# Kernel tuning notes

Measured on AMD Instinct MI355X. Metric: run time of the kernel, lower is better.

Reference implementation:

```python
import jax, jax.numpy as jnp
import numpy as np

B, C, H, W = 8, 256, 64, 64
CI = 128  # inter_channels = in_channels // reduction

def _conv1x1(x, w, b):
    # x: [b, c, h, w], w: [o, c], b: [o]
    return jnp.einsum('bchw,oc->bohw', x, w) + b[None, :, None, None]

def setup_inputs() -> dict:
    key = jax.random.key(0)
    ks = jax.random.split(key, 5)
    s_in = 1.0 / np.sqrt(C)
    s_ci = 1.0 / np.sqrt(CI)
    return {
        'x': jax.random.normal(ks[0], (B, C, H, W), jnp.float32),
        'w_g': jax.random.normal(ks[1], (CI, C), jnp.float32) * s_in,
        'b_g': jnp.zeros((CI,), jnp.float32),
        'w_theta': jax.random.normal(ks[2], (CI, C), jnp.float32) * s_in,
        'b_theta': jnp.zeros((CI,), jnp.float32),
        'w_phi': jax.random.normal(ks[3], (CI, C), jnp.float32) * s_in,
        'b_phi': jnp.zeros((CI,), jnp.float32),
        'w_out': jax.random.normal(ks[4], (C, CI), jnp.float32) * s_ci,
        'b_out': jnp.zeros((C,), jnp.float32),
    }

def reference(x, w_g, b_g, w_theta, b_theta, w_phi, b_phi, w_out, b_out):
    n, c, h, w = x.shape
    N = h * w
    g_x = _conv1x1(x, w_g, b_g).reshape(n, CI, N).transpose(0, 2, 1)        # [b, N, ci]
    theta_x = _conv1x1(x, w_theta, b_theta).reshape(n, CI, N).transpose(0, 2, 1)  # [b, N, ci]
    phi_x = _conv1x1(x, w_phi, b_phi).reshape(n, CI, N)                     # [b, ci, N]
    pw = jnp.einsum('bnc,bcm->bnm', theta_x, phi_x)                         # [b, N, N]
    # Faithful to source: divides by ci**(-0.5) == multiplies by sqrt(ci)
    pw = pw / (jnp.asarray(CI, x.dtype) ** -0.5)
    pw = jax.nn.softmax(pw, axis=-1)
    y = jnp.einsum('bnm,bmc->bnc', pw, g_x)                                 # [b, N, ci]
    y = y.transpose(0, 2, 1).reshape(n, CI, h, w)
    return x + _conv1x1(y, w_out, b_out)
```

## Files before the change

### kernel.cpp

```cpp
#include <hip/hip_runtime.h>
#include <hip/hip_bf16.h>
#include <stdint.h>
#include <stddef.h>


typedef __bf16 bf16;
typedef __attribute__((ext_vector_type(8))) __bf16 bf16x8;
typedef __attribute__((ext_vector_type(4))) __bf16 bf16x4;
typedef __attribute__((ext_vector_type(4))) float  f32x4;
typedef __attribute__((ext_vector_type(4))) int    i32x4;

#define MFMA16(a, b, c) __builtin_amdgcn_mfma_f32_16x16x32_bf16((a), (b), (c), 0, 0, 0)

__device__ __forceinline__ void gload_lds16(const void* g, void* l) {
    __builtin_amdgcn_global_load_lds(
        (const __attribute__((address_space(1))) void*)g,
        (__attribute__((address_space(3))) void*)l, 16, 0, 0);
}

constexpr int NB  = 8;
constexpr int NC  = 256;
constexpr int NN  = 4096;
constexpr int NCI = 128;
constexpr size_t NEL = (size_t)NB * NN * NCI;
constexpr int PBATCH = NN * NCI;

#define QSCALE (11.313708498984761f * 1.4426950408889634f)


__global__ __launch_bounds__(256) void k_proj3(
    const float* __restrict__ x,
    const float* __restrict__ wt, const float* __restrict__ bt,
    const float* __restrict__ wp, const float* __restrict__ bp,
    const float* __restrict__ wg, const float* __restrict__ bg,
    const float* __restrict__ wo, bf16* __restrict__ wob,
    bf16* __restrict__ qh, bf16* __restrict__ ql,
    bf16* __restrict__ kh, bf16* __restrict__ kl,
    bf16* __restrict__ vv)
{
    const int nt  = blockIdx.x;
    const int b   = blockIdx.y;
    const int tid = threadIdx.x;
    const int wv  = tid >> 6;
    const int ln  = tid & 63;
    const int lg  = ln >> 4;
    const int lq  = ln & 15;

    if (wob != nullptr && tid < 16) {
        int idx = (b * 64 + nt) * 64 + tid * 4;
        f32x4 w4 = *(const f32x4*)(wo + idx);
        bf16x4 o4;
#pragma unroll
        for (int e = 0; e < 4; ++e) o4[e] = (bf16)w4[e];
        *(bf16x4*)(wob + idx) = o4;
    }

    __shared__ char lds[49152];
    char* Ah = lds;
    char* Al = lds + 8192;
    char* Wh = lds + 16384;
    char* Wl = lds + 32768;

    f32x4 acc[3][8];
#pragma unroll
    for (int pj = 0; pj < 3; ++pj)
#pragma unroll
        for (int j = 0; j < 8; ++j) acc[pj][j] = f32x4{0.f, 0.f, 0.f, 0.f};

    const int n0 = nt * 64;

    for (int c0 = 0; c0 < NC; c0 += 64) {
        __syncthreads();
#pragma unroll
        for (int p = 0; p < 4; ++p) {
            int cc = p * 16 + (tid >> 4);
            int nn = (tid & 15) * 4;
            f32x4 xv = *(const f32x4*)(x + ((size_t)b * NC + (c0 + cc)) * NN + n0 + nn);
#pragma unroll
            for (int e = 0; e < 4; ++e) {
                float f = xv[e];
                bf16 hh = (bf16)f;
                int row = nn + e;
                int off = (row * 128 + cc * 2) ^ ((row & 7) << 4);
                *(bf16*)(Ah + off) = hh;
                *(bf16*)(Al + off) = (bf16)(f - (float)hh);
            }
        }

#pragma unroll
        for (int pj = 0; pj < 3; ++pj) {
            const float* W = (pj == 0) ? wt : (pj == 1) ? wp : wg;
            const bool split = (pj != 2);
            if (pj != 0) __syncthreads();
#pragma unroll
            for (int p = 0; p < 8; ++p) {
                int i  = p * 16 + (tid >> 4);
                int c4 = (tid & 15) * 4;
                f32x4 w4 = *(const f32x4*)(W + (size_t)i * NC + c0 + c4);
                bf16x4 hv, lv;
#pragma unroll
                for (int e = 0; e < 4; ++e) {
                    bf16 hh = (bf16)w4[e];
                    hv[e] = hh;
                    lv[e] = (bf16)(w4[e] - (float)hh);
                }
                int off = (i * 128 + c4 * 2) ^ ((i & 7) << 4);
                *(bf16x4*)(Wh + off) = hv;
                if (split) *(bf16x4*)(Wl + off) = lv;
            }
            __syncthreads();
#pragma unroll
            for (int kk = 0; kk < 2; ++kk) {
                int row  = wv * 16 + lq;
                int koff = kk * 64 + lg * 16;
                int aoff = (row * 128 + koff) ^ ((row & 7) << 4);
                bf16x8 ah = *(const bf16x8*)(Ah + aoff);
                bf16x8 al = *(const bf16x8*)(Al + aoff);
#pragma unroll
                for (int j = 0; j < 8; ++j) {
                    int ir   = j * 16 + lq;
                    int woff = (ir * 128 + koff) ^ ((ir & 7) << 4);
                    bf16x8 bh = *(const bf16x8*)(Wh + woff);
                    acc[pj][j] = MFMA16(ah, bh, acc[pj][j]);
                    if (split) {
                        bf16x8 bl = *(const bf16x8*)(Wl + woff);
                        acc[pj][j] = MFMA16(ah, bl, acc[pj][j]);
                        acc[pj][j] = MFMA16(al, bh, acc[pj][j]);
                    }
                }
            }
        }
    }

#pragma unroll
    for (int j = 0; j < 8; ++j) {
        int i = j * 16 + lq;
        float bvt = bt[i];
        float bvp = bp[i];
#pragma unroll
        for (int r = 0; r < 4; ++r) {
            int q = n0 + wv * 16 + lg * 4 + r;
            size_t off = ((size_t)b * NN + q) * NCI + i;
            float vt2 = (acc[0][j][r] + bvt) * QSCALE;
            bf16 th = (bf16)vt2;
            qh[off] = th; ql[off] = (bf16)(vt2 - (float)th);
            float vp2 = acc[1][j][r] + bvp;
            bf16 phh = (bf16)vp2;
            size_t ko = (size_t)b * PBATCH + (size_t)(q >> 5) * 4096
                      + (size_t)((q & 31) * 128 + (((i >> 3) ^ (q & 7)) << 3) + (i & 7));
            kh[ko] = phh; kl[ko] = (bf16)(vp2 - (float)phh);
        }
    }

    __syncthreads();
    char* T = lds;
#pragma unroll
    for (int j = 0; j < 8; ++j) {
        int i = j * 16 + lq;
        float bv2 = bg[i];
#pragma unroll
        for (int r = 0; r < 4; ++r) {
            int nl = wv * 16 + lg * 4 + r;
            int off = (i * 128 + nl * 2) ^ ((i & 7) << 4);
            *(bf16*)(T + off) = (bf16)(acc[2][j][r] + bv2);
        }
    }
    __syncthreads();
#pragma unroll
    for (int p = 0; p < 4; ++p) {
        int i  = p * 32 + (tid >> 3);
        int sl = tid & 7;
        i32x4 tv = *(const i32x4*)(T + ((i * 128 + sl * 16) ^ ((i & 7) << 4)));
        size_t off = (size_t)b * PBATCH
                   + (size_t)((((nt * 8 + (i >> 4)) * 2 + (sl >> 2)) * 64
                               + (sl & 3) * 16 + (i & 15)) * 8);
        *(i32x4*)(vv + off) = tv;
    }
}

__global__ __launch_bounds__(128, 2) void k_attn_sp(
    const bf16* __restrict__ qh, const bf16* __restrict__ ql,
    const bf16* __restrict__ khp, const bf16* __restrict__ klp,
    const bf16* __restrict__ vf,
    bf16* __restrict__ p0, bf16* __restrict__ p1, float* __restrict__ ml)
{
    const int bid = blockIdx.x;
    const int b   = bid & 7;
    const int rs  = bid >> 3;
    const int qt  = rs & 63;
    const int h   = rs >> 6;
    const int tid = threadIdx.x;
    const int wv  = tid >> 6;
    const int ln  = tid & 63;
    const int lg  = ln >> 4;
    const int lq  = ln & 15;
    const int n0  = qt * 64;
    bf16* ph = h ? p1 : p0;

    __shared__ __attribute__((aligned(16))) char lds[36864];
    char* P = lds + 32768 + wv * 2048;

    const bf16* ksh = khp + (size_t)b * PBATCH + wv * 2048 + (size_t)ln * 8;
    const bf16* ksl = klp + (size_t)b * PBATCH + wv * 2048 + (size_t)ln * 8;

    bf16x8 qhf[2][4], qlf[2][4];
#pragma unroll
    for (int q2 = 0; q2 < 2; ++q2) {
        int qrow = n0 + wv * 32 + q2 * 16 + lq;
        const bf16* bh = qh + ((size_t)b * NN + qrow) * NCI;
        const bf16* bl = ql + ((size_t)b * NN + qrow) * NCI;
#pragma unroll
        for (int kk = 0; kk < 4; ++kk) {
            qhf[q2][kk] = *(const bf16x8*)(bh + kk * 32 + lg * 8);
            qlf[q2][kk] = *(const bf16x8*)(bl + kk * 32 + lg * 8);
        }
    }

    f32x4 o[2][8];
#pragma unroll
    for (int q2 = 0; q2 < 2; ++q2)
#pragma unroll
        for (int j = 0; j < 8; ++j) o[q2][j] = f32x4{0.f, 0.f, 0.f, 0.f};
    float mrun[2] = {-1e30f, -1e30f};
    float lrun[2] = {0.f, 0.f};

    const bf16* vb = vf + (size_t)b * PBATCH + (size_t)ln * 8;

    {
        const bf16* sh = ksh + (size_t)(h * 64) * 4096;
        const bf16* sl = ksl + (size_t)(h * 64) * 4096;
        char* dh = lds + wv * 4096;
        char* dl = lds + 8192 + wv * 4096;
#pragma unroll
        for (int c = 0; c < 4; ++c) {
            gload_lds16(sh + c * 512, dh + c * 1024);
            gload_lds16(sl + c * 512, dl + c * 1024);
        }
    }
    __syncthreads();

    for (int t = 0; t < 64; ++t) {
        const int cur = t & 1;
        char* KHc = lds + cur * 16384;
        char* KLc = KHc + 8192;
        char* KHn = lds + (cur ^ 1) * 16384;
        char* KLn = KHn + 8192;
        const bool pre = (t < 63);

        if (pre) {
            const bf16* sh = ksh + (size_t)(h * 64 + t + 1) * 4096;
            const bf16* sl = ksl + (size_t)(h * 64 + t + 1) * 4096;
            char* dh = KHn + wv * 4096;
            char* dl = KLn + wv * 4096;
#pragma unroll
            for (int c = 0; c < 4; ++c) {
                gload_lds16(sh + c * 512, dh + c * 1024);
                gload_lds16(sl + c * 512, dl + c * 1024);
            }
        }
        __builtin_amdgcn_sched_barrier(0);

        f32x4 s[2][2];
        __builtin_amdgcn_s_setprio(1);
#pragma unroll
        for (int jm = 0; jm < 2; ++jm) {
            s[jm][0] = f32x4{0.f, 0.f, 0.f, 0.f};
            s[jm][1] = f32x4{0.f, 0.f, 0.f, 0.f};
            const int mrow = jm * 16 + lq;
            const int sw = (mrow & 7) << 4;
#pragma unroll
            for (int kk = 0; kk < 4; ++kk) {
                int aoff = (mrow * 256 + kk * 64 + lg * 16) ^ sw;
                bf16x8 ah = *(const bf16x8*)(KHc + aoff);
                bf16x8 al = *(const bf16x8*)(KLc + aoff);
                s[jm][0] = MFMA16(ah, qhf[0][kk], s[jm][0]);
                s[jm][1] = MFMA16(ah, qhf[1][kk], s[jm][1]);
                s[jm][0] = MFMA16(al, qhf[0][kk], s[jm][0]);
                s[jm][1] = MFMA16(al, qhf[1][kk], s[jm][1]);
                s[jm][0] = MFMA16(ah, qlf[0][kk], s[jm][0]);
                s[jm][1] = MFMA16(ah, qlf[1][kk], s[jm][1]);
            }
        }
        __builtin_amdgcn_s_setprio(0);

        bf16x8 bv[8];
        {
            const bf16* vp = vb + (size_t)(h * 32 + (t >> 1)) * 8192;
#pragma unroll
            for (int j = 0; j < 8; ++j)
                bv[j] = *(const bf16x8*)(vp + (j * 2 + (t & 1)) * 512);
        }
        __builtin_amdgcn_sched_barrier(0);

        float tm[2];
        tm[0] = s[0][0][0];
        tm[1] = s[0][1][0];
#pragma unroll
        for (int jm = 0; jm < 2; ++jm)
#pragma unroll
            for (int r = 0; r < 4; ++r) {
                tm[0] = fmaxf(tm[0], s[jm][0][r]);
                tm[1] = fmaxf(tm[1], s[jm][1][r]);
            }
#pragma unroll
        for (int q2 = 0; q2 < 2; ++q2) {
            tm[q2] = fmaxf(tm[q2], __shfl_xor(tm[q2], 16));
            tm[q2] = fmaxf(tm[q2], __shfl_xor(tm[q2], 32));
        }

        bool grow = (tm[0] > mrun[0] + 8.f) || (tm[1] > mrun[1] + 8.f);
        if (__any(grow)) {
            float alpha[2];
#pragma unroll
            for (int q2 = 0; q2 < 2; ++q2) {
                float mnew = fmaxf(mrun[q2], tm[q2]);
                alpha[q2] = exp2f(mrun[q2] - mnew);
                mrun[q2] = mnew;
                lrun[q2] *= alpha[q2];
            }
            float av0[4], av1[4];
#pragma unroll
            for (int r = 0; r < 4; ++r) {
                av0[r] = __shfl(alpha[0], lg * 4 + r);
                av1[r] = __shfl(alpha[1], lg * 4 + r);
            }
#pragma unroll
            for (int j = 0; j < 8; ++j)
#pragma unroll
                for (int r = 0; r < 4; ++r) {
                    o[0][j][r] *= av0[r];
                    o[1][j][r] *= av1[r];
                }
        }

        float psum[2] = {0.f, 0.f};
#pragma unroll
        for (int jm = 0; jm < 2; ++jm)
#pragma unroll
            for (int q2 = 0; q2 < 2; ++q2) {
                bf16x4 pk;
#pragma unroll
                for (int r = 0; r < 4; ++r) {
                    float e2 = exp2f(s[jm][q2][r] - mrun[q2]);
                    psum[q2] += e2;
                    pk[r] = (bf16)e2;
                }
                int row = q2 * 16 + lq;
                int off = (row * 64 + (jm * 16 + lg * 4) * 2) ^ ((row & 7) << 4);
                *(bf16x4*)(P + off) = pk;
            }
#pragma unroll
        for (int q2 = 0; q2 < 2; ++q2) {
            psum[q2] += __shfl_xor(psum[q2], 16);
            psum[q2] += __shfl_xor(psum[q2], 32);
            lrun[q2] += psum[q2];
        }

        bf16x8 pa[2];
#pragma unroll
        for (int q2 = 0; q2 < 2; ++q2) {
            int row = q2 * 16 + lq;
            pa[q2] = *(const bf16x8*)(P + ((row * 64 + lg * 16) ^ ((row & 7) << 4)));
        }
        __builtin_amdgcn_s_setprio(1);
#pragma unroll
        for (int j = 0; j < 8; ++j) {
            o[0][j] = MFMA16(pa[0], bv[j], o[0][j]);
            o[1][j] = MFMA16(pa[1], bv[j], o[1][j]);
        }
        __builtin_amdgcn_s_setprio(0);

        __syncthreads();
    }

    float rl0[4], rl1[4];
#pragma unroll
    for (int r = 0; r < 4; ++r) {
        rl0[r] = 1.f / __shfl(lrun[0], lg * 4 + r);
        rl1[r] = 1.f / __shfl(lrun[1], lg * 4 + r);
    }
#pragma unroll
    for (int j = 0; j < 8; ++j) {
        int d = j * 16 + lq;
#pragma unroll
        for (int r = 0; r < 4; ++r) {
            int q0 = n0 + wv * 32 + lg * 4 + r;
            ph[((size_t)b * NN + q0) * NCI + d]      = (bf16)(o[0][j][r] * rl0[r]);
            ph[((size_t)b * NN + q0 + 16) * NCI + d] = (bf16)(o[1][j][r] * rl1[r]);
        }
    }
    if (lg == 0) {
#pragma unroll
        for (int q2 = 0; q2 < 2; ++q2) {
            int row = n0 + wv * 32 + q2 * 16 + lq;
            size_t base = ((size_t)b * NN + row) * 4 + h * 2;
            ml[base]     = mrun[q2];
            ml[base + 1] = lrun[q2];
        }
    }
}

__global__ __launch_bounds__(256) void k_out(
    const bf16* __restrict__ p0, const bf16* __restrict__ p1,
    const float* __restrict__ ml, const float* __restrict__ x,
    const float* __restrict__ w_out, const bf16* __restrict__ wob,
    const float* __restrict__ b_out, float* __restrict__ out)
{
    const int nt  = blockIdx.x;
    const int b   = blockIdx.y;
    const int tid = threadIdx.x;
    const int wv  = tid >> 6;
    const int ln  = tid & 63;
    const int lg  = ln >> 4;
    const int lq  = ln & 15;
    const int n0  = nt * 64;

    __shared__ char Y[16384];
#pragma unroll
    for (int p = 0; p < 4; ++p) {
        int nn = p * 16 + (tid >> 4);
        int d0 = (tid & 15) * 8;
        size_t row = (size_t)b * NN + n0 + nn;
        f32x4 q = *(const f32x4*)(ml + row * 4);
        float M  = fmaxf(q[0], q[2]);
        float w0 = exp2f(q[0] - M) * q[1];
        float w1 = exp2f(q[2] - M) * q[3];
        float inv = 1.f / (w0 + w1);
        w0 *= inv; w1 *= inv;
        size_t off = row * NCI + d0;
        bf16x8 a = *(const bf16x8*)(p0 + off);
        bf16x8 c = *(const bf16x8*)(p1 + off);
        bf16x8 rr;
#pragma unroll
        for (int e = 0; e < 8; ++e)
            rr[e] = (bf16)(w0 * (float)a[e] + w1 * (float)c[e]);
        *(bf16x8*)(Y + ((nn * 256 + d0 * 2) ^ ((nn & 7) << 4))) = rr;
    }
    __syncthreads();

    bf16x8 af[4];
    {
        int row = wv * 16 + lq;
#pragma unroll
        for (int kk = 0; kk < 4; ++kk) {
            int koff = kk * 64 + lg * 16;
            af[kk] = *(const bf16x8*)(Y + ((row * 256 + koff) ^ ((row & 7) << 4)));
        }
    }

    f32x4 acc[16];
#pragma unroll
    for (int j = 0; j < 16; ++j) acc[j] = f32x4{0.f, 0.f, 0.f, 0.f};

    if (wob != nullptr) {
#pragma unroll
        for (int j = 0; j < 16; ++j) {
            int c = j * 16 + lq;
#pragma unroll
            for (int kk = 0; kk < 4; ++kk) {
                int i0 = kk * 32 + lg * 8;
                bf16x8 bw = *(const bf16x8*)(wob + (size_t)c * NCI + i0);
                acc[j] = MFMA16(af[kk], bw, acc[j]);
            }
        }
    } else {
#pragma unroll
        for (int j = 0; j < 16; ++j) {
            int c = j * 16 + lq;
#pragma unroll
            for (int kk = 0; kk < 4; ++kk) {
                int i0 = kk * 32 + lg * 8;
                f32x4 wa = *(const f32x4*)(w_out + (size_t)c * NCI + i0);
                f32x4 wb = *(const f32x4*)(w_out + (size_t)c * NCI + i0 + 4);
                bf16x8 bw;
#pragma unroll
                for (int e = 0; e < 4; ++e) { bw[e] = (bf16)wa[e]; bw[e + 4] = (bf16)wb[e]; }
                acc[j] = MFMA16(af[kk], bw, acc[j]);
            }
        }
    }

#pragma unroll
    for (int j = 0; j < 16; ++j) {
        int c = j * 16 + lq;
        int nb = n0 + wv * 16 + lg * 4;
        size_t off = ((size_t)b * NC + c) * (size_t)NN + nb;
        f32x4 xv = *(const f32x4*)(x + off);
        float bo = b_out[c];
        f32x4 r;
#pragma unroll
        for (int t = 0; t < 4; ++t) r[t] = acc[j][t] + xv[t] + bo;
        *(f32x4*)(out + off) = r;
    }
}

extern "C" void kernel_launch(void* const* d_in, const int* in_sizes, int n_in,
                              void* d_out, int out_size, void* d_ws, size_t ws_size,
                              hipStream_t stream)
{
    (void)in_sizes; (void)n_in; (void)out_size;
    const float* x  = (const float*)d_in[0];
    const float* wg = (const float*)d_in[1];
    const float* bg = (const float*)d_in[2];
    const float* wt = (const float*)d_in[3];
    const float* bt = (const float*)d_in[4];
    const float* wp = (const float*)d_in[5];
    const float* bp = (const float*)d_in[6];
    const float* wo = (const float*)d_in[7];
    const float* bo = (const float*)d_in[8];
    float* out = (float*)d_out;

    char* ws = (char*)d_ws;
    bf16* qh = (bf16*)(ws);
    bf16* ql = (bf16*)(ws + NEL * 2);
    bf16* kh = (bf16*)(ws + NEL * 4);
    bf16* kl = (bf16*)(ws + NEL * 6);
    bf16* vv = (bf16*)(ws + NEL * 8);
    bf16* p0 = (bf16*)(ws + NEL * 10);
    bf16* p1 = (bf16*)(ws + NEL * 12);
    float* ml = (float*)(ws + NEL * 14);
    const size_t ml_bytes = (size_t)NB * NN * 4 * sizeof(float);
    bf16* wob = nullptr;
    if (ws_size >= NEL * 14 + ml_bytes + (size_t)NC * NCI * sizeof(bf16))
        wob = (bf16*)(ws + NEL * 14 + ml_bytes);

    k_proj3<<<dim3(64, 8), 256, 0, stream>>>(x, wt, bt, wp, bp, wg, bg,
                                             wo, wob, qh, ql, kh, kl, vv);
    k_attn_sp<<<dim3(1024), 128, 0, stream>>>(qh, ql, kh, kl, vv, p0, p1, ml);
    k_out<<<dim3(64, 8), 256, 0, stream>>>(p0, p1, ml, x, wo, wob, bo, out);
}
```

Measured before the change: 236.6 us.

## Split key range across waves per block and merge partial softmax in LDS

The attention kernel now gives each block 32 queries instead of 64, and splits its half of the key range between the two waves. Each wave loads its own key tiles into a private LDS buffer, so the per-iteration __syncthreads is replaced by a wave-local vmcnt wait. After the loop, wave 1's partial output and running max/sum are merged into wave 0's through LDS using the online-softmax rescale. The grid doubles to 2048 blocks to give more parallelism and remove block-wide barriers. The cost is single-buffered loads that only partly overlap with compute, twice as many Q loads overall, and an extra merge pass.

After: 295.4 us. 24.8% more time.

```diff
diff --git a/kernel.cpp b/kernel.cpp
--- a/kernel.cpp
+++ b/kernel.cpp
@@ -186,27 +186,31 @@
 {
     const int bid = blockIdx.x;
     const int b   = bid & 7;
-    const int rs  = bid >> 3;
-    const int qt  = rs & 63;
-    const int h   = rs >> 6;
+    const int r2  = bid >> 3;
+    const int qt  = r2 & 127;
+    const int h   = r2 >> 7;
     const int tid = threadIdx.x;
     const int wv  = tid >> 6;
     const int ln  = tid & 63;
     const int lg  = ln >> 4;
     const int lq  = ln & 15;
-    const int n0  = qt * 64;
+    const int n0  = qt * 32;
     bf16* ph = h ? p1 : p0;
 
     __shared__ __attribute__((aligned(16))) char lds[36864];
-    char* P = lds + 32768 + wv * 2048;
-
-    const bf16* ksh = khp + (size_t)b * PBATCH + wv * 2048 + (size_t)ln * 8;
-    const bf16* ksl = klp + (size_t)b * PBATCH + wv * 2048 + (size_t)ln * 8;
+    char* KB = lds + wv * 16384;
+    char* KH = KB;
+    char* KL = KB + 8192;
+    char* P  = lds + 32768 + wv * 2048;
+
+    const int tb0 = h * 64 + wv * 32;
+    const bf16* ksh = khp + (size_t)b * PBATCH + (size_t)ln * 8;
+    const bf16* ksl = klp + (size_t)b * PBATCH + (size_t)ln * 8;
 
     bf16x8 qhf[2][4], qlf[2][4];
 #pragma unroll
     for (int q2 = 0; q2 < 2; ++q2) {
-        int qrow = n0 + wv * 32 + q2 * 16 + lq;
+        int qrow = n0 + q2 * 16 + lq;
         const bf16* bh = qh + ((size_t)b * NN + qrow) * NCI;
         const bf16* bl = ql + ((size_t)b * NN + qrow) * NCI;
 #pragma unroll
@@ -225,39 +229,20 @@
     float lrun[2] = {0.f, 0.f};
 
     const bf16* vb = vf + (size_t)b * PBATCH + (size_t)ln * 8;
+    const int v64 = h * 32 + wv * 16;
 
     {
-        const bf16* sh = ksh + (size_t)(h * 64) * 4096;
-        const bf16* sl = ksl + (size_t)(h * 64) * 4096;
-        char* dh = lds + wv * 4096;
-        char* dl = lds + 8192 + wv * 4096;
-#pragma unroll
-        for (int c = 0; c < 4; ++c) {
-            gload_lds16(sh + c * 512, dh + c * 1024);
-            gload_lds16(sl + c * 512, dl + c * 1024);
-        }
-    }
-    __syncthreads();
-
-    for (int t = 0; t < 64; ++t) {
-        const int cur = t & 1;
-        char* KHc = lds + cur * 16384;
-        char* KLc = KHc + 8192;
-        char* KHn = lds + (cur ^ 1) * 16384;
-        char* KLn = KHn + 8192;
-        const bool pre = (t < 63);
-
-        if (pre) {
-            const bf16* sh = ksh + (size_t)(h * 64 + t + 1) * 4096;
-            const bf16* sl = ksl + (size_t)(h * 64 + t + 1) * 4096;
-            char* dh = KHn + wv * 4096;
-            char* dl = KLn + wv * 4096;
-#pragma unroll
-            for (int c = 0; c < 4; ++c) {
-                gload_lds16(sh + c * 512, dh + c * 1024);
-                gload_lds16(sl + c * 512, dl + c * 1024);
-            }
-        }
+        const bf16* sh = ksh + (size_t)tb0 * 4096;
+        const bf16* sl = ksl + (size_t)tb0 * 4096;
+#pragma unroll
+        for (int c = 0; c < 8; ++c) {
+            gload_lds16(sh + c * 512, KH + c * 1024);
+            gload_lds16(sl + c * 512, KL + c * 1024);
+        }
+    }
+
+    for (int t = 0; t < 32; ++t) {
+        asm volatile("s_waitcnt vmcnt(0)" ::: "memory");
         __builtin_amdgcn_sched_barrier(0);
 
         f32x4 s[2][2];
@@ -271,8 +256,8 @@
 #pragma unroll
             for (int kk = 0; kk < 4; ++kk) {
                 int aoff = (mrow * 256 + kk * 64 + lg * 16) ^ sw;
-                bf16x8 ah = *(const bf16x8*)(KHc + aoff);
-                bf16x8 al = *(const bf16x8*)(KLc + aoff);
+                bf16x8 ah = *(const bf16x8*)(KH + aoff);
+                bf16x8 al = *(const bf16x8*)(KL + aoff);
                 s[jm][0] = MFMA16(ah, qhf[0][kk], s[jm][0]);
                 s[jm][1] = MFMA16(ah, qhf[1][kk], s[jm][1]);
                 s[jm][0] = MFMA16(al, qhf[0][kk], s[jm][0]);
@@ -285,10 +270,20 @@
 
         bf16x8 bv[8];
         {
-            const bf16* vp = vb + (size_t)(h * 32 + (t >> 1)) * 8192;
+            const bf16* vp = vb + (size_t)(v64 + (t >> 1)) * 8192;
 #pragma unroll
             for (int j = 0; j < 8; ++j)
                 bv[j] = *(const bf16x8*)(vp + (j * 2 + (t & 1)) * 512);
+        }
+
+        if (t < 31) {
+            const bf16* sh = ksh + (size_t)(tb0 + t + 1) * 4096;
+            const bf16* sl = ksl + (size_t)(tb0 + t + 1) * 4096;
+#pragma unroll
+            for (int c = 0; c < 8; ++c) {
+                gload_lds16(sh + c * 512, KH + c * 1024);
+                gload_lds16(sl + c * 512, KL + c * 1024);
+            }
         }
         __builtin_amdgcn_sched_barrier(0);
 
@@ -369,33 +364,61 @@
             o[1][j] = MFMA16(pa[1], bv[j], o[1][j]);
         }
         __builtin_amdgcn_s_setprio(0);
-
-        __syncthreads();
-    }
-
-    float rl0[4], rl1[4];
-#pragma unroll
-    for (int r = 0; r < 4; ++r) {
-        rl0[r] = 1.f / __shfl(lrun[0], lg * 4 + r);
-        rl1[r] = 1.f / __shfl(lrun[1], lg * 4 + r);
-    }
-#pragma unroll
-    for (int j = 0; j < 8; ++j) {
-        int d = j * 16 + lq;
-#pragma unroll
-        for (int r = 0; r < 4; ++r) {
-            int q0 = n0 + wv * 32 + lg * 4 + r;
-            ph[((size_t)b * NN + q0) * NCI + d]      = (bf16)(o[0][j][r] * rl0[r]);
-            ph[((size_t)b * NN + q0 + 16) * NCI + d] = (bf16)(o[1][j][r] * rl1[r]);
-        }
-    }
-    if (lg == 0) {
+    }
+
+    __syncthreads();
+    if (wv == 1) {
+#pragma unroll
+        for (int q2 = 0; q2 < 2; ++q2)
+#pragma unroll
+            for (int j = 0; j < 8; ++j)
+                *(f32x4*)(lds + (((q2 * 8 + j) * 64 + ln) << 4)) = o[q2][j];
+        f32x4 st;
+        st[0] = mrun[0]; st[1] = mrun[1]; st[2] = lrun[0]; st[3] = lrun[1];
+        *(f32x4*)(lds + 32768 + ln * 16) = st;
+    }
+    __syncthreads();
+    if (wv == 0) {
+        f32x4 st = *(const f32x4*)(lds + 32768 + ln * 16);
+        float w0[2], w1[2], lm[2], Mm[2];
 #pragma unroll
         for (int q2 = 0; q2 < 2; ++q2) {
-            int row = n0 + wv * 32 + q2 * 16 + lq;
-            size_t base = ((size_t)b * NN + row) * 4 + h * 2;
-            ml[base]     = mrun[q2];
-            ml[base + 1] = lrun[q2];
+            float M = fmaxf(mrun[q2], st[q2]);
+            w0[q2] = exp2f(mrun[q2] - M);
+            w1[q2] = exp2f(st[q2] - M);
+            lm[q2] = lrun[q2] * w0[q2] + st[2 + q2] * w1[q2];
+            Mm[q2] = M;
+        }
+        float a0[2][4], a1[2][4], rl[2][4];
+#pragma unroll
+        for (int q2 = 0; q2 < 2; ++q2)
+#pragma unroll
+            for (int r = 0; r < 4; ++r) {
+                a0[q2][r] = __shfl(w0[q2], lg * 4 + r);
+                a1[q2][r] = __shfl(w1[q2], lg * 4 + r);
+                rl[q2][r] = 1.f / __shfl(lm[q2], lg * 4 + r);
+            }
+#pragma unroll
+        for (int q2 = 0; q2 < 2; ++q2)
+#pragma unroll
+            for (int j = 0; j < 8; ++j) {
+                f32x4 o1 = *(const f32x4*)(lds + (((q2 * 8 + j) * 64 + ln) << 4));
+                int d = j * 16 + lq;
+#pragma unroll
+                for (int r = 0; r < 4; ++r) {
+                    int q0 = n0 + q2 * 16 + lg * 4 + r;
+                    float val = (o[q2][j][r] * a0[q2][r] + o1[r] * a1[q2][r]) * rl[q2][r];
+                    ph[((size_t)b * NN + q0) * NCI + d] = (bf16)val;
+                }
+            }
+        if (lg == 0) {
+#pragma unroll
+            for (int q2 = 0; q2 < 2; ++q2) {
+                int row = n0 + q2 * 16 + lq;
+                size_t base = ((size_t)b * NN + row) * 4 + h * 2;
+                ml[base]     = Mm[q2];
+                ml[base + 1] = lm[q2];
+            }
         }
     }
 }
@@ -526,6 +549,6 @@
 
     k_proj3<<<dim3(64, 8), 256, 0, stream>>>(x, wt, bt, wp, bp, wg, bg,
                                              wo, wob, qh, ql, kh, kl, vv);
-    k_attn_sp<<<dim3(1024), 128, 0, stream>>>(qh, ql, kh, kl, vv, p0, p1, ml);
+    k_attn_sp<<<dim3(2048), 128, 0, stream>>>(qh, ql, kh, kl, vv, p0, p1, ml);
     k_out<<<dim3(64, 8), 256, 0, stream>>>(p0, p1, ml, x, wo, wob, bo, out);
 }
```
